# Kernel tuning notes

Measured on AMD Instinct MI355X. Metric: run time of the kernel, lower is better.

Reference implementation:

```python
import jax, jax.numpy as jnp
import numpy as np

EMB_DIM = 2048
N_Q_HEADS = 32
N_KV_HEADS = 8
HEAD_DIM = EMB_DIM // N_Q_HEADS  # 64
N_REP = N_Q_HEADS // N_KV_HEADS  # 4
ROPE_BASE = 10000.0


def setup_inputs() -> dict:
    key = jax.random.key(0)
    ks = jax.random.split(key, 9)
    B, T = 2, 2048
    kv_dim = HEAD_DIM * N_KV_HEADS
    s = 0.02
    return {
        "x":  jax.random.normal(ks[0], (B, T, EMB_DIM), jnp.float32),
        "Wq": jax.random.normal(ks[1], (EMB_DIM, EMB_DIM), jnp.float32) * s,
        "bq": jax.random.normal(ks[2], (EMB_DIM,), jnp.float32) * s,
        "Wk": jax.random.normal(ks[3], (kv_dim, EMB_DIM), jnp.float32) * s,
        "bk": jax.random.normal(ks[4], (kv_dim,), jnp.float32) * s,
        "Wv": jax.random.normal(ks[5], (kv_dim, EMB_DIM), jnp.float32) * s,
        "bv": jax.random.normal(ks[6], (kv_dim,), jnp.float32) * s,
        "Wo": jax.random.normal(ks[7], (EMB_DIM, EMB_DIM), jnp.float32) * s,
        "bo": jax.random.normal(ks[8], (EMB_DIM,), jnp.float32) * s,
    }


def _rope_tables(T, D, dtype):
    inv_freq = 1.0 / (ROPE_BASE ** (jnp.arange(0, D, 2, dtype=jnp.float32) / D))
    t = jnp.arange(T, dtype=jnp.float32)
    freqs = jnp.einsum("i,j->ij", t, inv_freq)          # [T, D/2]
    emb = jnp.concatenate([freqs, freqs], axis=-1)       # [T, D]
    # broadcast over batch and heads: [1, T, 1, D]
    return jnp.cos(emb)[None, :, None, :].astype(dtype), jnp.sin(emb)[None, :, None, :].astype(dtype)


def _rotate_half(x):
    x1, x2 = jnp.split(x, 2, axis=-1)
    return jnp.concatenate([-x2, x1], axis=-1)


def reference(x, Wq, bq, Wk, bk, Wv, bv, Wo, bo):
    B, T, C = x.shape
    q = (x @ Wq.T + bq).reshape(B, T, N_Q_HEADS, HEAD_DIM)
    k = (x @ Wk.T + bk).reshape(B, T, N_KV_HEADS, HEAD_DIM)
    v = (x @ Wv.T + bv).reshape(B, T, N_KV_HEADS, HEAD_DIM)

    cos, sin = _rope_tables(T, HEAD_DIM, x.dtype)
    q = q * cos + _rotate_half(q) * sin
    k = k * cos + _rotate_half(k) * sin

    q = q.transpose(0, 2, 1, 3)                          # [B, Hq, T, D]
    k = k.transpose(0, 2, 1, 3)                          # [B, Hkv, T, D]
    v = v.transpose(0, 2, 1, 3)
    # GQA: repeat_interleave kv heads to match query heads
    k = jnp.repeat(k, N_REP, axis=1)                     # [B, Hq, T, D]
    v = jnp.repeat(v, N_REP, axis=1)

    scale = 1.0 / jnp.sqrt(jnp.asarray(HEAD_DIM, x.dtype))
    att = jnp.einsum("bhqd,bhkd->bhqk", q, k) * scale    # [B, Hq, T, T]
    causal = jnp.tril(jnp.ones((T, T), dtype=bool))
    att = jnp.where(causal[None, None], att, -jnp.inf)
    att = jax.nn.softmax(att, axis=-1)

    y = jnp.einsum("bhqk,bhkd->bhqd", att, v)            # [B, Hq, T, D]
    y = y.transpose(0, 2, 1, 3).reshape(B, T, C)
    return y @ Wo.T + bo
```

## Files before the change

### kernel.cpp

```cpp
#include <hip/hip_runtime.h>
#include <hip/hip_bf16.h>
#include <math.h>


typedef __attribute__((ext_vector_type(8))) short short8;
typedef __attribute__((ext_vector_type(4))) float f32x4;

#define MFMA16(a,b,c) __builtin_amdgcn_mfma_f32_16x16x32_bf16((a),(b),(c),0,0,0)

__device__ __forceinline__ ushort f2bf(float f) {
  union { float f; unsigned u; } x; x.f = f;
  unsigned r = x.u + 0x7fffu + ((x.u >> 16) & 1u);
  return (ushort)(r >> 16);
}
__device__ __forceinline__ float bf2f(ushort h) {
  union { unsigned u; float f; } x; x.u = ((unsigned)h) << 16;
  return x.f;
}
__device__ __forceinline__ uint pkbf(float a, float b) {
  union { float f; unsigned u; } x, y; x.f = a; y.f = b;
  return ((x.u + 0x8000u) >> 16) | ((y.u + 0x8000u) & 0xffff0000u);
}

__device__ __forceinline__ void g2l16(const void* g, void* l) {
  __builtin_amdgcn_global_load_lds(
      (__attribute__((address_space(1))) void*)g,
      (__attribute__((address_space(3))) void*)l, 16, 0, 0);
}

__global__ void cvt_all(const float* __restrict__ x,  const float* __restrict__ wq,
                        const float* __restrict__ wk, const float* __restrict__ wv,
                        const float* __restrict__ wo,
                        ushort* __restrict__ x_bf, ushort* __restrict__ wqkv,
                        ushort* __restrict__ wo_bf) {
  int i = blockIdx.x * 256 + threadIdx.x;
  const float4* src; ushort* dst; int off;
  if (i < 2097152)      { src = (const float4*)x;  dst = x_bf;             off = i; }
  else if (i < 3145728) { src = (const float4*)wq; dst = wqkv;             off = i - 2097152; }
  else if (i < 3407872) { src = (const float4*)wk; dst = wqkv + 4194304;   off = i - 3145728; }
  else if (i < 3670016) { src = (const float4*)wv; dst = wqkv + 5242880;   off = i - 3407872; }
  else                  { src = (const float4*)wo; dst = wo_bf;            off = i - 3670016; }
  float4 v = src[off];
  ushort4 o;
  o.x = f2bf(v.x); o.y = f2bf(v.y); o.z = f2bf(v.z); o.w = f2bf(v.w);
  ((ushort4*)dst)[off] = o;
}

template<int OUT_BF16>
__global__ __launch_bounds__(256, 3)
void gemm128(const ushort* __restrict__ A, const ushort* __restrict__ Bw,
             const float* __restrict__ b0, const float* __restrict__ b1,
             const float* __restrict__ b2, int nb1, int nb2,
             void* __restrict__ Cout, int M, int N, int K) {
  __shared__ ushort As[2][128*32];
  __shared__ ushort Bs[2][128*32];
  const int tid = threadIdx.x;
  const int wave = tid >> 6, lane = tid & 63;
  const int wm = wave >> 1, wn = wave & 1;
  const int quad = lane >> 4, l16 = lane & 15;
  const int swg = (l16 >> 1) & 3;
  const int m0 = blockIdx.y * 128, n0 = blockIdx.x * 128;

  f32x4 acc[4][4] = {};

  auto stage = [&](int buf, int k0) {
#pragma unroll
    for (int i = 0; i < 2; ++i) {
      int cbase = (i*4 + wave) * 64;
      int p = cbase + lane;
      int row = p >> 2, pcb = p & 3;
      int cl = pcb ^ ((row >> 1) & 3);
      g2l16(A  + (size_t)(m0 + row) * K + k0 + cl * 8, As[buf] + (size_t)cbase * 8);
      g2l16(Bw + (size_t)(n0 + row) * K + k0 + cl * 8, Bs[buf] + (size_t)cbase * 8);
    }
  };

  stage(0, 0);
  for (int k0 = 0; k0 < K; k0 += 32) {
    __syncthreads();
    int cur = (k0 >> 5) & 1;
    if (k0 + 32 < K) stage(cur ^ 1, k0 + 32);

    short8 af[4], bfr[4];
#pragma unroll
    for (int mi = 0; mi < 4; ++mi)
      af[mi] = *(const short8*)(As[cur] + (wm*64 + mi*16 + l16)*32 + ((quad ^ swg) * 8));
#pragma unroll
    for (int ni = 0; ni < 4; ++ni)
      bfr[ni] = *(const short8*)(Bs[cur] + (wn*64 + ni*16 + l16)*32 + ((quad ^ swg) * 8));
#pragma unroll
    for (int mi = 0; mi < 4; ++mi)
#pragma unroll
      for (int ni = 0; ni < 4; ++ni)
        acc[mi][ni] = MFMA16(af[mi], bfr[ni], acc[mi][ni]);
  }

#pragma unroll
  for (int ni = 0; ni < 4; ++ni) {
    int n = n0 + wn*64 + ni*16 + l16;
    float bias = (n < nb1) ? b0[n] : ((n < nb2) ? b1[n - nb1] : b2[n - nb2]);
#pragma unroll
    for (int mi = 0; mi < 4; ++mi) {
#pragma unroll
      for (int r = 0; r < 4; ++r) {
        int m = m0 + wm*64 + mi*16 + quad*4 + r;
        float v = acc[mi][ni][r] + bias;
        if (OUT_BF16) ((ushort*)Cout)[(size_t)m * N + n] = f2bf(v);
        else          ((float*)Cout)[(size_t)m * N + n] = v;
      }
    }
  }
}

#define QSCALE 0.18033688011112043f
__global__ void rope_scatter(const ushort* __restrict__ qkv,
                             ushort* __restrict__ qr, ushort* __restrict__ kr) {
  int i = blockIdx.x * 256 + threadIdx.x;
  int j = i & 31;
  int rest = i >> 5;
  int hh = rest % 40;
  int mrow = rest / 40;
  int t = mrow & 2047, b = mrow >> 11;
  float freq = (float)t * exp2f((float)j * (-13.28771237954945f / 32.0f));
  float sn = sinf(freq), cs = cosf(freq);
  const ushort* row = qkv + (size_t)mrow * 3072;
  if (hh < 32) {
    float x1 = bf2f(row[hh*64 + j]);
    float x2 = bf2f(row[hh*64 + 32 + j]);
    ushort* dst = qr + ((size_t)(b*32 + hh) * 2048 + t) * 64 + j;
    dst[0]  = f2bf((x1*cs - x2*sn) * QSCALE);
    dst[32] = f2bf((x2*cs + x1*sn) * QSCALE);
  } else {
    int hk = hh - 32;
    float x1 = bf2f(row[2048 + hk*64 + j]);
    float x2 = bf2f(row[2048 + hk*64 + 32 + j]);
    ushort* dst = kr + ((size_t)(b*8 + hk) * 2048 + t) * 64 + j;
    dst[0]  = f2bf(x1*cs - x2*sn);
    dst[32] = f2bf(x2*cs + x1*sn);
  }
}

__global__ void v_transpose(const ushort* __restrict__ qkv, ushort* __restrict__ vt) {
  __shared__ ushort tile[64*65];
  int t0 = blockIdx.x * 64;
  int hk = blockIdx.y;
  int b  = blockIdx.z;
  int tid = threadIdx.x;
#pragma unroll
  for (int i = 0; i < 16; ++i) {
    int e = i * 256 + tid;
    int r = e >> 6, c = e & 63;
    tile[r*65 + c] = qkv[(size_t)(b*2048 + t0 + r) * 3072 + 2560 + hk*64 + c];
  }
  __syncthreads();
#pragma unroll
  for (int i = 0; i < 16; ++i) {
    int e = i * 256 + tid;
    int d = e >> 6, c = e & 63;
    vt[((size_t)(b*8 + hk) * 64 + d) * 2048 + t0 + c] = tile[c*65 + d];
  }
}

__global__ __launch_bounds__(256, 4)
void attn(const ushort* __restrict__ Q, const ushort* __restrict__ Kb,
          const ushort* __restrict__ Vt, ushort* __restrict__ Y) {
  __shared__ ushort Ks[2][64*64];
  __shared__ ushort Vs[2][64*64];
  __shared__ ushort Ps[4*16*64];
  const int tid = threadIdx.x, wave = tid >> 6, lane = tid & 63;
  const int quad = lane >> 4, l16 = lane & 15;
  const int h = blockIdx.y, b = blockIdx.z;
  const int hk = h >> 2;
  const ushort* Qb = Q  + ((size_t)(b*32 + h)  * 2048) * 64;
  const ushort* Kg = Kb + ((size_t)(b*8 + hk) * 2048) * 64;
  const ushort* Vg = Vt + ((size_t)(b*8 + hk) * 64) * 2048;
  ushort* Pw = Ps + wave * 1024;
  const int sw = l16 & 7;

  auto stage = [&](int buf, int kt) {
#pragma unroll
    for (int i = 0; i < 2; ++i) {
      int cbase = (i*4 + wave) * 64;
      int p = cbase + lane;
      int row = p >> 3, pcb = p & 7;
      int cl = pcb ^ (row & 7);
      g2l16(Kg + (size_t)(kt*64 + row)*64 + cl*8, Ks[buf] + (size_t)cbase*8);
      g2l16(Vg + (size_t)row*2048 + kt*64 + cl*8, Vs[buf] + (size_t)cbase*8);
    }
  };

  for (int pass = 0; pass < 2; ++pass) {
    const int qt = pass ? (31 - blockIdx.x) : blockIdx.x;
    const int q0 = qt * 64;
    const int qrow = q0 + wave*16 + l16;
    short8 qf0 = *(const short8*)(Qb + (size_t)qrow*64 + quad*8);
    short8 qf1 = *(const short8*)(Qb + (size_t)qrow*64 + 32 + quad*8);

    f32x4 o[4] = {};
    f32x4 l4 = {0.f, 0.f, 0.f, 0.f};

    __syncthreads();
    stage(0, 0);

    for (int kt = 0; kt <= qt; ++kt) {
      __syncthreads();
      int cur = kt & 1;
      if (kt < qt) stage(cur ^ 1, kt + 1);

      f32x4 s[4];
#pragma unroll
      for (int kb = 0; kb < 4; ++kb) {
        const ushort* krow = Ks[cur] + (kb*16 + l16)*64;
        short8 kf0 = *(const short8*)(krow + ((quad       ^ sw) * 8));
        short8 kf1 = *(const short8*)(krow + (((4 + quad) ^ sw) * 8));
        f32x4 z = {0.f, 0.f, 0.f, 0.f};
        z = MFMA16(kf0, qf0, z);
        s[kb] = MFMA16(kf1, qf1, z);
      }

      if (kt == qt) {
        int ql = wave*16 + l16;
#pragma unroll
        for (int kb = 0; kb < 4; ++kb) {
          int keyl = kb*16 + quad*4;
#pragma unroll
          for (int r = 0; r < 4; ++r)
            if (keyl + r > ql) s[kb][r] = -INFINITY;
        }
      }

#pragma unroll
      for (int kb = 0; kb < 4; ++kb)
#pragma unroll
        for (int r = 0; r < 4; ++r)
          s[kb][r] = __builtin_amdgcn_exp2f(s[kb][r]);

      l4 += (s[0] + s[1]) + (s[2] + s[3]);

#pragma unroll
      for (int kb = 0; kb < 4; ++kb) {
        uint2 pk;
        pk.x = pkbf(s[kb][0], s[kb][1]);
        pk.y = pkbf(s[kb][2], s[kb][3]);
        int G = (kb*2 + (quad >> 1)) ^ sw;
        *(uint2*)((char*)Pw + l16*128 + G*16 + (quad & 1)*8) = pk;
      }

#pragma unroll
      for (int kc = 0; kc < 2; ++kc) {
        short8 pf = *(const short8*)((char*)Pw + l16*128 + (((kc*4 + quad) ^ sw) * 16));
#pragma unroll
        for (int db = 0; db < 4; ++db) {
          const ushort* vrow = Vs[cur] + (db*16 + l16)*64;
          short8 vf = *(const short8*)(vrow + (((kc*4 + quad) ^ sw) * 8));
          o[db] = MFMA16(vf, pf, o[db]);
        }
      }
    }

    float l = (l4[0] + l4[1]) + (l4[2] + l4[3]);
    l += __shfl_xor(l, 16);
    l += __shfl_xor(l, 32);
    float inv = 1.0f / l;

    int q = q0 + wave*16 + l16;
#pragma unroll
    for (int db = 0; db < 4; ++db) {
      size_t base = ((size_t)(b*2048 + q)) * 2048 + h*64 + db*16 + quad*4;
      ((uint*)Y)[base >> 1]       = pkbf(o[db][0]*inv, o[db][1]*inv);
      ((uint*)Y)[(base >> 1) + 1] = pkbf(o[db][2]*inv, o[db][3]*inv);
    }
  }
}

extern "C" void kernel_launch(void* const* d_in, const int* in_sizes, int n_in,
                              void* d_out, int out_size, void* d_ws, size_t ws_size,
                              hipStream_t stream) {
  (void)in_sizes; (void)n_in; (void)out_size; (void)ws_size;
  const float* x  = (const float*)d_in[0];
  const float* Wq = (const float*)d_in[1];
  const float* bq = (const float*)d_in[2];
  const float* Wk = (const float*)d_in[3];
  const float* bk = (const float*)d_in[4];
  const float* Wv = (const float*)d_in[5];
  const float* bv = (const float*)d_in[6];
  const float* Wo = (const float*)d_in[7];
  const float* bo = (const float*)d_in[8];
  float* out = (float*)d_out;

  ushort* ws    = (ushort*)d_ws;
  ushort* x_bf  = ws;
  ushort* wqkv  = x_bf + 8388608;
  ushort* wo_bf = wqkv + 6291456;
  ushort* qkv   = wo_bf + 4194304;
  ushort* qr    = qkv + 12582912;
  ushort* kr    = qr + 8388608;
  ushort* vt    = kr + 2097152;
  ushort* Y     = x_bf;

  cvt_all<<<18432, 256, 0, stream>>>(x, Wq, Wk, Wv, Wo, x_bf, wqkv, wo_bf);
  gemm128<1><<<dim3(24, 32), 256, 0, stream>>>(x_bf, wqkv, bq, bk, bv, 2048, 2560,
                                               qkv, 4096, 3072, 2048);
  rope_scatter<<<20480, 256, 0, stream>>>(qkv, qr, kr);
  v_transpose<<<dim3(32, 8, 2), 256, 0, stream>>>(qkv, vt);
  attn<<<dim3(16, 32, 2), 256, 0, stream>>>(qr, kr, vt, Y);
  gemm128<0><<<dim3(16, 32), 256, 0, stream>>>(Y, wo_bf, bo, bo, bo, 1<<30, 1<<30,
                                               out, 4096, 2048, 2048);
}
```

Measured before the change: 305.0 us.

## Fuse RoPE and V transpose into QKV GEMM epilogue

The QKV projection GEMM now applies bias, rotary embedding and the Q scale in its epilogue, writing Q and K directly in head-major layout and V in transposed layout. This removes the separate rope_scatter and v_transpose kernels and the intermediate qkv buffer round trip through memory. The epilogue uses fast __sinf/__cosf intrinsics and scattered 2-byte stores, which may reduce accuracy for large angles and lower store efficiency.

```diff
diff --git a/kernel.cpp b/kernel.cpp
--- a/kernel.cpp
+++ b/kernel.cpp
@@ -7,15 +7,13 @@
 typedef __attribute__((ext_vector_type(4))) float f32x4;
 
 #define MFMA16(a,b,c) __builtin_amdgcn_mfma_f32_16x16x32_bf16((a),(b),(c),0,0,0)
+#define QSCALE 0.18033688011112043f
+#define NFREQ  (-13.28771237954945f / 32.0f)
 
 __device__ __forceinline__ ushort f2bf(float f) {
   union { float f; unsigned u; } x; x.f = f;
   unsigned r = x.u + 0x7fffu + ((x.u >> 16) & 1u);
   return (ushort)(r >> 16);
-}
-__device__ __forceinline__ float bf2f(ushort h) {
-  union { unsigned u; float f; } x; x.u = ((unsigned)h) << 16;
-  return x.f;
 }
 __device__ __forceinline__ uint pkbf(float a, float b) {
   union { float f; unsigned u; } x, y; x.f = a; y.f = b;
@@ -46,12 +44,13 @@
   ((ushort4*)dst)[off] = o;
 }
 
-template<int OUT_BF16>
 __global__ __launch_bounds__(256, 3)
-void gemm128(const ushort* __restrict__ A, const ushort* __restrict__ Bw,
-             const float* __restrict__ b0, const float* __restrict__ b1,
-             const float* __restrict__ b2, int nb1, int nb2,
-             void* __restrict__ Cout, int M, int N, int K) {
+void gemm_qkv(const ushort* __restrict__ A, const ushort* __restrict__ Bw,
+              const float* __restrict__ bq, const float* __restrict__ bk,
+              const float* __restrict__ bv,
+              ushort* __restrict__ qr, ushort* __restrict__ kr,
+              ushort* __restrict__ vt) {
+  const int K = 2048;
   __shared__ ushort As[2][128*32];
   __shared__ ushort Bs[2][128*32];
   const int tid = threadIdx.x;
@@ -95,69 +94,118 @@
         acc[mi][ni] = MFMA16(af[mi], bfr[ni], acc[mi][ni]);
   }
 
+  const int bb = m0 >> 11;
+  const int tb = (m0 & 2047) + wm*64;
+
+  if (blockIdx.x < 20) {
+    const bool isq = blockIdx.x < 16;
+    const float scale = isq ? QSCALE : 1.0f;
+#pragma unroll
+    for (int ni = 0; ni < 2; ++ni) {
+      int n = n0 + wn*64 + ni*16 + l16;
+      int d = ni*16 + l16;
+      float bias1, bias2;
+      ushort* dst;
+      if (isq) {
+        bias1 = bq[n]; bias2 = bq[n + 32];
+        dst = qr + ((size_t)(bb*32 + (n >> 6)) * 2048) * 64 + d;
+      } else {
+        bias1 = bk[n - 2048]; bias2 = bk[n - 2016];
+        dst = kr + ((size_t)(bb*8 + ((n >> 6) - 32)) * 2048) * 64 + d;
+      }
+      float invf = exp2f((float)d * NFREQ);
+#pragma unroll
+      for (int mi = 0; mi < 4; ++mi) {
+#pragma unroll
+        for (int r = 0; r < 4; ++r) {
+          int t = tb + mi*16 + quad*4 + r;
+          float x1 = acc[mi][ni][r]   + bias1;
+          float x2 = acc[mi][ni+2][r] + bias2;
+          float f = (float)t * invf;
+          float sn = __sinf(f), cs = __cosf(f);
+          dst[(size_t)t*64]      = f2bf((x1*cs - x2*sn) * scale);
+          dst[(size_t)t*64 + 32] = f2bf((x2*cs + x1*sn) * scale);
+        }
+      }
+    }
+  } else {
+#pragma unroll
+    for (int ni = 0; ni < 4; ++ni) {
+      int n = n0 + wn*64 + ni*16 + l16;
+      int d = ni*16 + l16;
+      float bias = bv[n - 2560];
+      ushort* dst = vt + ((size_t)(bb*8 + ((n - 2560) >> 6)) * 64 + d) * 2048;
+#pragma unroll
+      for (int mi = 0; mi < 4; ++mi) {
+        int t = tb + mi*16 + quad*4;
+        uint2 pk;
+        pk.x = (uint)f2bf(acc[mi][ni][0]+bias) | ((uint)f2bf(acc[mi][ni][1]+bias) << 16);
+        pk.y = (uint)f2bf(acc[mi][ni][2]+bias) | ((uint)f2bf(acc[mi][ni][3]+bias) << 16);
+        *(uint2*)(dst + t) = pk;
+      }
+    }
+  }
+}
+
+__global__ __launch_bounds__(256, 3)
+void gemm128(const ushort* __restrict__ A, const ushort* __restrict__ Bw,
+             const float* __restrict__ b0,
+             float* __restrict__ Cout, int M, int N, int K) {
+  __shared__ ushort As[2][128*32];
+  __shared__ ushort Bs[2][128*32];
+  const int tid = threadIdx.x;
+  const int wave = tid >> 6, lane = tid & 63;
+  const int wm = wave >> 1, wn = wave & 1;
+  const int quad = lane >> 4, l16 = lane & 15;
+  const int swg = (l16 >> 1) & 3;
+  const int m0 = blockIdx.y * 128, n0 = blockIdx.x * 128;
+
+  f32x4 acc[4][4] = {};
+
+  auto stage = [&](int buf, int k0) {
+#pragma unroll
+    for (int i = 0; i < 2; ++i) {
+      int cbase = (i*4 + wave) * 64;
+      int p = cbase + lane;
+      int row = p >> 2, pcb = p & 3;
+      int cl = pcb ^ ((row >> 1) & 3);
+      g2l16(A  + (size_t)(m0 + row) * K + k0 + cl * 8, As[buf] + (size_t)cbase * 8);
+      g2l16(Bw + (size_t)(n0 + row) * K + k0 + cl * 8, Bs[buf] + (size_t)cbase * 8);
+    }
+  };
+
+  stage(0, 0);
+  for (int k0 = 0; k0 < K; k0 += 32) {
+    __syncthreads();
+    int cur = (k0 >> 5) & 1;
+    if (k0 + 32 < K) stage(cur ^ 1, k0 + 32);
+
+    short8 af[4], bfr[4];
+#pragma unroll
+    for (int mi = 0; mi < 4; ++mi)
+      af[mi] = *(const short8*)(As[cur] + (wm*64 + mi*16 + l16)*32 + ((quad ^ swg) * 8));
+#pragma unroll
+    for (int ni = 0; ni < 4; ++ni)
+      bfr[ni] = *(const short8*)(Bs[cur] + (wn*64 + ni*16 + l16)*32 + ((quad ^ swg) * 8));
+#pragma unroll
+    for (int mi = 0; mi < 4; ++mi)
+#pragma unroll
+      for (int ni = 0; ni < 4; ++ni)
+        acc[mi][ni] = MFMA16(af[mi], bfr[ni], acc[mi][ni]);
+  }
+
 #pragma unroll
   for (int ni = 0; ni < 4; ++ni) {
     int n = n0 + wn*64 + ni*16 + l16;
-    float bias = (n < nb1) ? b0[n] : ((n < nb2) ? b1[n - nb1] : b2[n - nb2]);
+    float bias = b0[n];
 #pragma unroll
     for (int mi = 0; mi < 4; ++mi) {
 #pragma unroll
       for (int r = 0; r < 4; ++r) {
         int m = m0 + wm*64 + mi*16 + quad*4 + r;
-        float v = acc[mi][ni][r] + bias;
-        if (OUT_BF16) ((ushort*)Cout)[(size_t)m * N + n] = f2bf(v);
-        else          ((float*)Cout)[(size_t)m * N + n] = v;
-      }
-    }
-  }
-}
-
-#define QSCALE 0.18033688011112043f
-__global__ void rope_scatter(const ushort* __restrict__ qkv,
-                             ushort* __restrict__ qr, ushort* __restrict__ kr) {
-  int i = blockIdx.x * 256 + threadIdx.x;
-  int j = i & 31;
-  int rest = i >> 5;
-  int hh = rest % 40;
-  int mrow = rest / 40;
-  int t = mrow & 2047, b = mrow >> 11;
-  float freq = (float)t * exp2f((float)j * (-13.28771237954945f / 32.0f));
-  float sn = sinf(freq), cs = cosf(freq);
-  const ushort* row = qkv + (size_t)mrow * 3072;
-  if (hh < 32) {
-    float x1 = bf2f(row[hh*64 + j]);
-    float x2 = bf2f(row[hh*64 + 32 + j]);
-    ushort* dst = qr + ((size_t)(b*32 + hh) * 2048 + t) * 64 + j;
-    dst[0]  = f2bf((x1*cs - x2*sn) * QSCALE);
-    dst[32] = f2bf((x2*cs + x1*sn) * QSCALE);
-  } else {
-    int hk = hh - 32;
-    float x1 = bf2f(row[2048 + hk*64 + j]);
-    float x2 = bf2f(row[2048 + hk*64 + 32 + j]);
-    ushort* dst = kr + ((size_t)(b*8 + hk) * 2048 + t) * 64 + j;
-    dst[0]  = f2bf(x1*cs - x2*sn);
-    dst[32] = f2bf(x2*cs + x1*sn);
-  }
-}
-
-__global__ void v_transpose(const ushort* __restrict__ qkv, ushort* __restrict__ vt) {
-  __shared__ ushort tile[64*65];
-  int t0 = blockIdx.x * 64;
-  int hk = blockIdx.y;
-  int b  = blockIdx.z;
-  int tid = threadIdx.x;
-#pragma unroll
-  for (int i = 0; i < 16; ++i) {
-    int e = i * 256 + tid;
-    int r = e >> 6, c = e & 63;
-    tile[r*65 + c] = qkv[(size_t)(b*2048 + t0 + r) * 3072 + 2560 + hk*64 + c];
-  }
-  __syncthreads();
-#pragma unroll
-  for (int i = 0; i < 16; ++i) {
-    int e = i * 256 + tid;
-    int d = e >> 6, c = e & 63;
-    vt[((size_t)(b*8 + hk) * 64 + d) * 2048 + t0 + c] = tile[c*65 + d];
+        Cout[(size_t)m * N + n] = acc[mi][ni][r] + bias;
+      }
+    }
   }
 }
 
@@ -292,18 +340,13 @@
   ushort* x_bf  = ws;
   ushort* wqkv  = x_bf + 8388608;
   ushort* wo_bf = wqkv + 6291456;
-  ushort* qkv   = wo_bf + 4194304;
-  ushort* qr    = qkv + 12582912;
+  ushort* qr    = wo_bf + 4194304;
   ushort* kr    = qr + 8388608;
   ushort* vt    = kr + 2097152;
   ushort* Y     = x_bf;
 
   cvt_all<<<18432, 256, 0, stream>>>(x, Wq, Wk, Wv, Wo, x_bf, wqkv, wo_bf);
-  gemm128<1><<<dim3(24, 32), 256, 0, stream>>>(x_bf, wqkv, bq, bk, bv, 2048, 2560,
-                                               qkv, 4096, 3072, 2048);
-  rope_scatter<<<20480, 256, 0, stream>>>(qkv, qr, kr);
-  v_transpose<<<dim3(32, 8, 2), 256, 0, stream>>>(qkv, vt);
+  gemm_qkv<<<dim3(24, 32), 256, 0, stream>>>(x_bf, wqkv, bq, bk, bv, qr, kr, vt);
   attn<<<dim3(16, 32, 2), 256, 0, stream>>>(qr, kr, vt, Y);
-  gemm128<0><<<dim3(16, 32), 256, 0, stream>>>(Y, wo_bf, bo, bo, bo, 1<<30, 1<<30,
-                                               out, 4096, 2048, 2048);
-}
+  gemm128<<<dim3(16, 32), 256, 0, stream>>>(Y, wo_bf, bo, out, 4096, 2048, 2048);
+}
```

New measurement: 302.3 us. No clear change (-0.9%).
